# Kernel tuning notes

Measured on AMD Instinct MI355X. Metric: run time of the kernel, lower is better.

Reference implementation:

```python
import jax, jax.numpy as jnp
import numpy as np

IN_DIM = 128
OUT_DIM = 128
D_MODEL = IN_DIM // 4        # mamba d_model = 32
D_STATE = 16
D_CONV = 4
EXPAND = 2
D_INNER = EXPAND * D_MODEL   # 64
DT_RANK = (D_MODEL + 15) // 16  # ceil(d_model/16) = 2
N_MIXERS = 3                 # shared + 2 experts (stacked on leading axis)
B, DD, HH, WW = 2, 16, 16, 16


def setup_inputs() -> dict:
    key = jax.random.key(0)
    ks = jax.random.split(key, 12)
    rn = lambda k, s, sc=0.05: jax.random.normal(k, s, dtype=jnp.float32) * sc
    M = N_MIXERS
    return {
        "x": jax.random.normal(ks[0], (B, IN_DIM, DD, HH, WW), dtype=jnp.float32),
        "dataset_id": jax.random.randint(ks[1], (B,), 0, 2),
        "ln_g": jnp.ones((M, IN_DIM), jnp.float32),
        "ln_b": jnp.zeros((M, IN_DIM), jnp.float32),
        "in_w": rn(ks[2], (M, 2 * D_INNER, D_MODEL)),
        "conv_w": rn(ks[3], (M, D_INNER, D_CONV), 0.2),
        "conv_b": rn(ks[4], (M, D_INNER), 0.1),
        "xp_w": rn(ks[5], (M, DT_RANK + 2 * D_STATE, D_INNER)),
        "dt_w": rn(ks[6], (M, D_INNER, DT_RANK), 0.2),
        "dt_b": rn(ks[7], (M, D_INNER), 0.1),
        "A_log": jnp.broadcast_to(jnp.log(jnp.arange(1, D_STATE + 1, dtype=jnp.float32)), (M, D_INNER, D_STATE)) + jnp.zeros((M, D_INNER, D_STATE), jnp.float32),
        "Dp": jnp.ones((M, D_INNER), jnp.float32),
        "out_w": rn(ks[8], (M, D_MODEL, D_INNER)),
        "proj_w": rn(ks[9], (M, OUT_DIM, IN_DIM)),
        "proj_b": jnp.zeros((M, OUT_DIM), jnp.float32),
        "skip": jnp.ones((M,), jnp.float32),
    }


def layernorm(x, g, b, eps=1e-5):
    mu = jnp.mean(x, -1, keepdims=True)
    var = jnp.mean((x - mu) ** 2, -1, keepdims=True)
    return (x - mu) * jax.lax.rsqrt(var + eps) * g + b


def mamba(xp, p):
    # Standard Mamba block: in_proj -> causal depthwise conv1d -> selective scan -> SiLU gate -> out_proj
    # xp: (B, L, d_model)
    Bb, L, _ = xp.shape
    xz = jnp.einsum('bld,ed->ble', xp, p["in_w"])            # (B,L,2*d_inner)
    xi, z = jnp.split(xz, 2, axis=-1)
    conv = jax.lax.conv_general_dilated(xi.transpose(0, 2, 1), p["conv_w"][:, None, :], (1,), [(D_CONV - 1, 0)], feature_group_count=D_INNER)
    xi = jax.nn.silu(conv + p["conv_b"][None, :, None]).transpose(0, 2, 1)  # (B,L,d_inner)
    dbc = jnp.einsum('bld,ed->ble', xi, p["xp_w"])
    dt_low = dbc[..., :DT_RANK]
    Bm = dbc[..., DT_RANK:DT_RANK + D_STATE]
    Cm = dbc[..., DT_RANK + D_STATE:]
    delta = jax.nn.softplus(jnp.einsum('blr,dr->bld', dt_low, p["dt_w"]) + p["dt_b"])  # (B,L,d_inner)
    A = -jnp.exp(p["A_log"])                                  # (d_inner, d_state)

    def step(h, inp):
        xt, dt, Bt, Ct = inp                                  # (B,di),(B,di),(B,ds),(B,ds)
        dA = jnp.exp(dt[..., None] * A)                       # (B,d_inner,d_state)
        h = dA * h + (dt * xt)[..., None] * Bt[:, None, :]
        return h, jnp.einsum('bds,bs->bd', h, Ct)

    h0 = jnp.zeros((Bb, D_INNER, D_STATE), xp.dtype)
    xs = (xi.transpose(1, 0, 2), delta.transpose(1, 0, 2), Bm.transpose(1, 0, 2), Cm.transpose(1, 0, 2))
    _, ys = jax.lax.scan(step, h0, xs)
    y = ys.transpose(1, 0, 2) + p["Dp"] * xi
    y = y * jax.nn.silu(z)
    return jnp.einsum('ble,de->bld', y, p["out_w"])


def mixer(x, p):
    # PetaloMixer pom_module='full': LN -> 4-way channel chunk -> shared Mamba + skip -> concat -> LN -> Linear
    Bb, C, Dd, Hh, Ww = x.shape
    L = Dd * Hh * Ww
    xf = x.reshape(Bb, C, L).transpose(0, 2, 1)               # (B,L,C)
    xn = layernorm(xf, p["ln_g"], p["ln_b"])
    parts = jnp.stack(jnp.split(xn, 4, axis=-1), 0)           # (4,B,L,d_model)
    outs = jax.vmap(lambda q: mamba(q, p))(parts) + p["skip"] * parts
    xm = jnp.concatenate([outs[i] for i in range(4)], -1)     # (B,L,C)
    xm = layernorm(xm, p["ln_g"], p["ln_b"])                  # same LayerNorm reused, as in torch code
    xpj = jnp.einsum('blc,oc->blo', xm, p["proj_w"]) + p["proj_b"]
    return xpj.transpose(0, 2, 1).reshape(Bb, OUT_DIM, Dd, Hh, Ww)


def _forward(x, dataset_id, params):
    shared = mixer(x, {k: v[0] for k, v in params.items()})
    # experts: compute both over full batch (vectorized), then per-sample select by dataset_id
    eouts = jax.vmap(lambda p: mixer(x, p))({k: v[1:] for k, v in params.items()})  # (2,B,out,D,H,W)
    ids = jnp.minimum(dataset_id, N_MIXERS - 2)               # clamp: min(m, n_experts-1)
    expert_out = eouts[ids, jnp.arange(x.shape[0])]
    return shared + expert_out                                # Dropout3d(p=0.2) is identity in eval mode


def reference(x, dataset_id, ln_g, ln_b, in_w, conv_w, conv_b, xp_w, dt_w, dt_b, A_log, Dp, out_w, proj_w, proj_b, skip):
    params = dict(ln_g=ln_g, ln_b=ln_b, in_w=in_w, conv_w=conv_w, conv_b=conv_b, xp_w=xp_w, dt_w=dt_w, dt_b=dt_b, A_log=A_log, Dp=Dp, out_w=out_w, proj_w=proj_w, proj_b=proj_b, skip=skip)
    return _forward(x, dataset_id, params)
```

## Files before the change

kernel.cpp:

```cpp
#include <hip/hip_runtime.h>
#include <math.h>

#define LSEQ 4096
#define CIN  128
#define DI   64
#define NS   16
#define NP   4
#define NJ   4
#define NSEQ 16
#define NC   128
#define LC   32
#define LOG2E 1.44269504f

__device__ __forceinline__ int mixer_of(const int* did, int j){
  if((j&1)==0) return 0;
  int d = did[j>>1];
  return 1 + (d < 1 ? d : 1);
}
__device__ __forceinline__ float silu_f(float x){ return x/(1.f+expf(-x)); }

__global__ __launch_bounds__(256) void k1_ln_inproj(
  const float* __restrict__ x, const int* __restrict__ did,
  const float* __restrict__ ln_g, const float* __restrict__ ln_b,
  const float* __restrict__ in_w,
  float* __restrict__ xnb, float* __restrict__ xzr, float* __restrict__ zb)
{
  const int j = blockIdx.y, b = j>>1, t = threadIdx.x;
  const int l0 = blockIdx.x*32;
  const int m = mixer_of(did, j);
  __shared__ float s_x[128][33];
  __shared__ float s_xn[32][132];
  __shared__ float s_mu[32], s_rs[32];

  for(int idx=t; idx<4096; idx+=256){
    int c = idx>>5, ll = idx&31;
    s_x[c][ll] = x[((size_t)b*CIN+c)*LSEQ + l0+ll];
  }
  float wreg[32];
  {
    const float4* wp = (const float4*)(in_w + (size_t)m*4096 + (size_t)(t&127)*32);
    #pragma unroll
    for(int i=0;i<8;i++){
      float4 v = wp[i];
      wreg[i*4+0]=v.x; wreg[i*4+1]=v.y; wreg[i*4+2]=v.z; wreg[i*4+3]=v.w;
    }
  }
  __syncthreads();

  {
    const int wv = t>>6, lane = t&63;
    const int g = lane&7, lw = lane>>3;
    const int ll = wv*8+lw;
    float sum=0.f;
    #pragma unroll
    for(int k=0;k<16;k++) sum += s_x[g*16+k][ll];
    sum += __shfl_xor(sum,1); sum += __shfl_xor(sum,2); sum += __shfl_xor(sum,4);
    float mu = sum*(1.f/128.f);
    float vs=0.f;
    #pragma unroll
    for(int k=0;k<16;k++){ float dv = s_x[g*16+k][ll]-mu; vs += dv*dv; }
    vs += __shfl_xor(vs,1); vs += __shfl_xor(vs,2); vs += __shfl_xor(vs,4);
    if(g==0){ s_mu[ll]=mu; s_rs[ll]=rsqrtf(vs*(1.f/128.f)+1e-5f); }
  }
  __syncthreads();

  for(int idx=t; idx<4096; idx+=256){
    int ll = idx>>7, c = idx&127;
    float xn = (s_x[c][ll]-s_mu[ll])*s_rs[ll]*ln_g[m*128+c] + ln_b[m*128+c];
    s_xn[ll][c] = xn;
    xnb[((size_t)j*LSEQ + l0+ll)*128 + c] = xn;
  }
  __syncthreads();

  const int e = t&127, hh = t>>7;
  for(int ll=hh*16; ll<hh*16+16; ++ll){
    #pragma unroll
    for(int q=0;q<4;q++){
      const float4* xr4 = (const float4*)(&s_xn[ll][q*32]);
      float acc=0.f;
      #pragma unroll
      for(int k4=0;k4<8;k4++){
        float4 xv = xr4[k4];
        acc += xv.x*wreg[k4*4+0] + xv.y*wreg[k4*4+1]
             + xv.z*wreg[k4*4+2] + xv.w*wreg[k4*4+3];
      }
      size_t base = ((size_t)(j*NP+q)*LSEQ + l0+ll)*64;
      if(e<64) xzr[base+e]=acc; else zb[base+e-64]=acc;
    }
  }
}

__global__ __launch_bounds__(256) void k2_conv_xproj(
  const int* __restrict__ did,
  const float* __restrict__ conv_w, const float* __restrict__ conv_b,
  const float* __restrict__ xp_w, const float* __restrict__ dt_w, const float* __restrict__ dt_b,
  const float* __restrict__ xzr, float* __restrict__ dxb,
  float* __restrict__ bmb, float* __restrict__ cmb)
{
  const int seq = blockIdx.y, j = seq>>2, t = threadIdx.x;
  const int l0 = blockIdx.x*32;
  const int m = mixer_of(did, j);
  const int d = t&63, r = t>>6;
  __shared__ float s_xi[32][64];
  __shared__ float s_dbc[32][2];
  __shared__ float s_cwT[4][64];
  __shared__ float s_cb[64], s_dtw[128], s_dtb[64];

  float lz[11];
  #pragma unroll
  for(int i=0;i<11;i++){
    int l = l0 + r*8 - 3 + i;
    lz[i] = (l>=0) ? xzr[((size_t)seq*LSEQ + l)*64 + d] : 0.f;
  }
  { int k=t>>6, dd=t&63; s_cwT[k][dd]=conv_w[m*256+dd*4+k]; }
  if(t<64){ s_cb[t]=conv_b[m*64+t]; s_dtb[t]=dt_b[m*64+t]; }
  if(t<128) s_dtw[t]=dt_w[m*128+t];
  __syncthreads();

  {
    float cw0=s_cwT[0][d], cw1=s_cwT[1][d], cw2=s_cwT[2][d], cw3=s_cwT[3][d], cb=s_cb[d];
    #pragma unroll
    for(int i=0;i<8;i++){
      float xc = cb + lz[i]*cw0 + lz[i+1]*cw1 + lz[i+2]*cw2 + lz[i+3]*cw3;
      s_xi[r*8+i][d] = silu_f(xc);
    }
  }

  float wreg[64];
  if(d<34){
    const float4* wp = (const float4*)(xp_w + (size_t)m*2176 + (size_t)d*64);
    #pragma unroll
    for(int k4=0;k4<16;k4++){
      float4 v = wp[k4];
      wreg[k4*4+0]=v.x; wreg[k4*4+1]=v.y; wreg[k4*4+2]=v.z; wreg[k4*4+3]=v.w;
    }
  }
  __syncthreads();

  if(d<34){
    #pragma unroll
    for(int ip=0; ip<4; ip++){
      int ll = r*8 + ip*2;
      const float4* xa=(const float4*)&s_xi[ll][0];
      const float4* xb=(const float4*)&s_xi[ll+1][0];
      float a0=0.f,a1=0.f,b0=0.f,b1=0.f;
      #pragma unroll
      for(int k=0;k<16;k+=2){
        float4 u=xa[k], u2=xa[k+1], v=xb[k], v2=xb[k+1];
        a0 += u.x *wreg[4*k+0]+u.y *wreg[4*k+1]+u.z *wreg[4*k+2]+u.w *wreg[4*k+3];
        a1 += u2.x*wreg[4*k+4]+u2.y*wreg[4*k+5]+u2.z*wreg[4*k+6]+u2.w*wreg[4*k+7];
        b0 += v.x *wreg[4*k+0]+v.y *wreg[4*k+1]+v.z *wreg[4*k+2]+v.w *wreg[4*k+3];
        b1 += v2.x*wreg[4*k+4]+v2.y*wreg[4*k+5]+v2.z*wreg[4*k+6]+v2.w*wreg[4*k+7];
      }
      float A=a0+a1, Bv=b0+b1;
      if(d<2){ s_dbc[ll][d]=A; s_dbc[ll+1][d]=Bv; }
      else if(d<18){
        bmb[((size_t)seq*LSEQ + l0+ll  )*16 + d-2]=A;
        bmb[((size_t)seq*LSEQ + l0+ll+1)*16 + d-2]=Bv;
      } else {
        cmb[((size_t)seq*LSEQ + l0+ll  )*16 + d-18]=A;
        cmb[((size_t)seq*LSEQ + l0+ll+1)*16 + d-18]=Bv;
      }
    }
  }
  __syncthreads();

  {
    float w0=s_dtw[d*2], w1=s_dtw[d*2+1], bb=s_dtb[d];
    #pragma unroll
    for(int i=0;i<8;i++){
      int ll=r*8+i;
      float dtv = s_dbc[ll][0]*w0 + s_dbc[ll][1]*w1 + bb;
      float dlv = dtv>20.f ? dtv : log1pf(expf(dtv));
      float2 pk; pk.x=dlv; pk.y=s_xi[ll][d];
      *(float2*)(dxb + ((size_t)seq*LSEQ + l0+ll)*128 + d*2) = pk;
    }
  }
}

__global__ __launch_bounds__(256) void k3a_scan_pe(
  const int* __restrict__ did, const float* __restrict__ A_log,
  const float* __restrict__ dxb, const float* __restrict__ bmb,
  float* __restrict__ pb, float* __restrict__ eb)
{
  const int seq=blockIdx.y, j=seq>>2, t=threadIdx.x;
  const int wave=t>>6, d=t&63;
  const int cl=wave>>1, sh=wave&1, sh8=sh*8;
  const int chunk=blockIdx.x*2+cl;
  const int l0=blockIdx.x*2*LC;
  const int m=mixer_of(did,j);
  __shared__ float s_b[2*LC*NS];
  ((float4*)s_b)[t] = ((const float4*)(bmb + ((size_t)seq*LSEQ + l0)*NS))[t];

  float as_h[8], as0;
  {
    const float* ap = A_log + (size_t)m*1024 + d*16;
    as0 = -expf(ap[0])*LOG2E;
    #pragma unroll
    for(int k=0;k<8;k++) as_h[k] = -expf(ap[sh8+k])*LOG2E;
  }
  bool stl = true;
  #pragma unroll
  for(int k=0;k<8;k++){ float ex=(float)(sh8+k+1)*as0; stl = stl && (fabsf(as_h[k]-ex) <= 1e-4f*fabsf(ex)); }
  const bool structured = (__ballot(stl) == ~0ull);

  const float2* dxp=(const float2*)(dxb + ((size_t)seq*LSEQ + (size_t)chunk*LC)*128);
  float E[8];
  #pragma unroll
  for(int k=0;k<8;k++) E[k]=0.f;
  float Sdl=0.f;
  __syncthreads();

  #define ASTEP(i_, dx_, FAST_) { \
    float dl=dx_.x, xv=dx_.y; float u=dl*xv; Sdl+=dl; \
    const float4* bq=(const float4*)(s_b + cl*(LC*NS) + (i_)*NS + sh8); \
    float4 b0=bq[0], b1=bq[1]; \
    float bb[8]={b0.x,b0.y,b0.z,b0.w, b1.x,b1.y,b1.z,b1.w}; \
    float p[8]; \
    if(FAST_){ float q=exp2f(dl*as0); p[0]=exp2f(dl*as_h[0]); \
      _Pragma("unroll") for(int k=1;k<8;k++) p[k]=p[k-1]*q; \
    } else { _Pragma("unroll") for(int k=0;k<8;k++) p[k]=exp2f(dl*as_h[k]); } \
    _Pragma("unroll") for(int k=0;k<8;k++) E[k]=fmaf(p[k],E[k],u*bb[k]); }

  #define ALOOP(FAST_) { \
    float2 dxw[4]; \
    _Pragma("unroll") for(int k=0;k<4;k++) dxw[k]=dxp[k*64+d]; \
    for(int ii=0;ii<LC;ii+=4){ \
      float2 c0=dxw[0],c1=dxw[1],c2=dxw[2],c3=dxw[3]; \
      if(ii+4<LC){ _Pragma("unroll") for(int k=0;k<4;k++) dxw[k]=dxp[(ii+4+k)*64+d]; } \
      ASTEP(ii+0,c0,FAST_); ASTEP(ii+1,c1,FAST_); ASTEP(ii+2,c2,FAST_); ASTEP(ii+3,c3,FAST_); } }

  if(structured){ ALOOP(1) } else { ALOOP(0) }
  #undef ALOOP
  #undef ASTEP

  float P[8];
  #pragma unroll
  for(int k=0;k<8;k++) P[k]=exp2f(Sdl*as_h[k]);
  size_t oo=(((size_t)seq*NC+chunk)*64+d)*16 + sh8;
  float4* pp=(float4*)(pb+oo); float4* ep=(float4*)(eb+oo);
  pp[0]=make_float4(P[0],P[1],P[2],P[3]);
  pp[1]=make_float4(P[4],P[5],P[6],P[7]);
  ep[0]=make_float4(E[0],E[1],E[2],E[3]);
  ep[1]=make_float4(E[4],E[5],E[6],E[7]);
}

__global__ __launch_bounds__(256) void k3b_combine(
  float* p_hs, const float* __restrict__ eb)
{
  const int seq=blockIdx.y, q=blockIdx.x, t=threadIdx.x;
  const size_t elem = (size_t)q*256+t;
  #define OFF(c_) (((size_t)seq*NC+(c_))*1024 + elem)
  float pA[16],eA[16],pB[16],eB[16];
  #pragma unroll
  for(int k=0;k<16;k++){ pA[k]=p_hs[OFF(k)]; eA[k]=eb[OFF(k)]; }
  float h=0.f;
  for(int bt=0; bt<8; bt+=2){
    if(bt+1<8){
      #pragma unroll
      for(int k=0;k<16;k++){ pB[k]=p_hs[OFF((bt+1)*16+k)]; eB[k]=eb[OFF((bt+1)*16+k)]; }
    }
    #pragma unroll
    for(int k=0;k<16;k++){ p_hs[OFF(bt*16+k)]=h; h=fmaf(pA[k],h,eA[k]); }
    if(bt+2<8){
      #pragma unroll
      for(int k=0;k<16;k++){ pA[k]=p_hs[OFF((bt+2)*16+k)]; eA[k]=eb[OFF((bt+2)*16+k)]; }
    }
    #pragma unroll
    for(int k=0;k<16;k++){ p_hs[OFF((bt+1)*16+k)]=h; h=fmaf(pB[k],h,eB[k]); }
  }
  #undef OFF
}

__global__ __launch_bounds__(256) void k3c4_scan_outproj(
  const int* __restrict__ did, const float* __restrict__ A_log, const float* __restrict__ Dp,
  const float* __restrict__ dxb,
  const float* __restrict__ bmb, const float* __restrict__ cmb,
  const float* __restrict__ zb, const float* __restrict__ hsb,
  const float* __restrict__ out_w, const float* __restrict__ skipv,
  const float* __restrict__ xnb, float* __restrict__ xmb)
{
  const int seq=blockIdx.y, j=seq>>2, p=seq&3, t=threadIdx.x;
  const int wave=t>>6, d=t&63;
  const int cl=wave>>1, sh=wave&1, sh8=sh*8;
  const int chunk=blockIdx.x*2+cl;
  const int l0=blockIdx.x*2*LC;
  const int m=mixer_of(did,j);
  __shared__ float s_b[2*LC*NS];
  __shared__ float s_c[2*LC*NS];
  __shared__ float s_y0[64*64];
  __shared__ float s_y1[64*64];
  {
    const float4* bsrc=(const float4*)(bmb + ((size_t)seq*LSEQ + l0)*NS);
    const float4* csrc=(const float4*)(cmb + ((size_t)seq*LSEQ + l0)*NS);
    ((float4*)s_b)[t]=bsrc[t];
    ((float4*)s_c)[t]=csrc[t];
  }
  float as_h[8], as0;
  {
    const float* ap = A_log + (size_t)m*1024 + d*16;
    as0 = -expf(ap[0])*LOG2E;
    #pragma unroll
    for(int k=0;k<8;k++) as_h[k] = -expf(ap[sh8+k])*LOG2E;
  }
  bool stl = true;
  #pragma unroll
  for(int k=0;k<8;k++){ float ex=(float)(sh8+k+1)*as0; stl = stl && (fabsf(as_h[k]-ex) <= 1e-4f*fabsf(ex)); }
  const bool structured = (__ballot(stl) == ~0ull);

  const float dpv2 = (sh==0) ? Dp[m*64+d] : 0.f;
  float h[8];
  {
    const float4* hp=(const float4*)(hsb + (((size_t)seq*NC+chunk)*64+d)*16 + sh8);
    float4 v0=hp[0], v1=hp[1];
    h[0]=v0.x; h[1]=v0.y; h[2]=v0.z; h[3]=v0.w;
    h[4]=v1.x; h[5]=v1.y; h[6]=v1.z; h[7]=v1.w;
  }
  const float2* dxp=(const float2*)(dxb + ((size_t)seq*LSEQ + (size_t)chunk*LC)*128);
  float* s_yw = sh ? s_y1 : s_y0;
  __syncthreads();

  #define CSTEP(i_, dx_, FAST_) { \
    float dl=dx_.x, xv=dx_.y; float u=dl*xv; \
    const float4* bq=(const float4*)(s_b + cl*(LC*NS) + (i_)*NS + sh8); \
    const float4* cq=(const float4*)(s_c + cl*(LC*NS) + (i_)*NS + sh8); \
    float4 b0=bq[0],b1=bq[1],c0=cq[0],c1=cq[1]; \
    float bb[8]={b0.x,b0.y,b0.z,b0.w, b1.x,b1.y,b1.z,b1.w}; \
    float cc[8]={c0.x,c0.y,c0.z,c0.w, c1.x,c1.y,c1.z,c1.w}; \
    float pz[8]; \
    if(FAST_){ float q=exp2f(dl*as0); pz[0]=exp2f(dl*as_h[0]); \
      _Pragma("unroll") for(int k=1;k<8;k++) pz[k]=pz[k-1]*q; \
    } else { _Pragma("unroll") for(int k=0;k<8;k++) pz[k]=exp2f(dl*as_h[k]); } \
    float ya=0.f, yb2=0.f; \
    _Pragma("unroll") for(int k=0;k<8;k++){ \
      h[k]=fmaf(pz[k],h[k],u*bb[k]); \
      float hv=h[k]*cc[k]; \
      if(k&1) yb2+=hv; else ya+=hv; } \
    float y=ya+yb2; y=fmaf(dpv2,xv,y); \
    s_yw[(cl*LC+(i_))*64 + d]=y; }

  #define CLOOP(FAST_) { \
    float2 dxw[4]; \
    _Pragma("unroll") for(int k=0;k<4;k++) dxw[k]=dxp[k*64+d]; \
    for(int ii=0;ii<LC;ii+=4){ \
      float2 c0w=dxw[0],c1w=dxw[1],c2w=dxw[2],c3w=dxw[3]; \
      if(ii+4<LC){ _Pragma("unroll") for(int k=0;k<4;k++) dxw[k]=dxp[(ii+4+k)*64+d]; } \
      CSTEP(ii+0,c0w,FAST_); CSTEP(ii+1,c1w,FAST_); CSTEP(ii+2,c2w,FAST_); CSTEP(ii+3,c3w,FAST_); } }

  if(structured){ CLOOP(1) } else { CLOOP(0) }
  #undef CLOOP
  #undef CSTEP

  __syncthreads();
  {
    const float* zp = zb + ((size_t)seq*LSEQ + l0)*64;
    #pragma unroll
    for(int it=0; it<16; ++it){
      int idx = t + it*256;
      float ysum = s_y0[idx] + s_y1[idx];
      s_y0[idx] = ysum * silu_f(zp[idx]);
    }
  }
  const int o=t&31, grp=t>>5;
  float wreg[64];
  {
    const float4* wp=(const float4*)(out_w + (size_t)m*2048 + (size_t)o*64);
    #pragma unroll
    for(int k4=0;k4<16;k4++){
      float4 v=wp[k4];
      wreg[k4*4+0]=v.x; wreg[k4*4+1]=v.y; wreg[k4*4+2]=v.z; wreg[k4*4+3]=v.w;
    }
  }
  const float sk=skipv[m];
  __syncthreads();
  for(int ll=grp; ll<64; ll+=8){
    const float4* ya=(const float4*)&s_y0[ll*64];
    float a0=0.f,a1=0.f;
    #pragma unroll
    for(int k=0;k<16;k+=2){
      float4 u=ya[k], u2=ya[k+1];
      a0 += u.x *wreg[4*k+0]+u.y *wreg[4*k+1]+u.z *wreg[4*k+2]+u.w *wreg[4*k+3];
      a1 += u2.x*wreg[4*k+4]+u2.y*wreg[4*k+5]+u2.z*wreg[4*k+6]+u2.w*wreg[4*k+7];
    }
    size_t xidx=((size_t)j*LSEQ + l0+ll)*128 + p*32 + o;
    xmb[xidx]=(a0+a1) + sk*xnb[xidx];
  }
}

__global__ __launch_bounds__(256) void k5_ln2_proj(
  const int* __restrict__ did, const float* __restrict__ ln_g, const float* __restrict__ ln_b,
  const float* __restrict__ proj_w, const float* __restrict__ proj_b,
  const float* __restrict__ xmb, float* __restrict__ out)
{
  const int b=blockIdx.y, l0=blockIdx.x*16, t=threadIdx.x;
  const int eh = t>>7, local = t&127;
  const int j = 2*b+eh;
  const int m = mixer_of(did, j);
  __shared__ float s_xn[2][16][132];
  __shared__ float s_comb[16][132];
  __shared__ float s_murs[2][16][2];

  for(int idx=local; idx<2048; idx+=128){
    int ll=idx>>7, c=idx&127;
    s_xn[eh][ll][c] = xmb[((size_t)j*LSEQ + l0+ll)*128 + c];
  }
  __syncthreads();
  {
    const int lane = t&63;
    const int g = lane&7, lw = lane>>3;
    const int ll = ((t>>6)&1)*8 + lw;
    float sum=0.f;
    #pragma unroll
    for(int k=0;k<16;k++) sum += s_xn[eh][ll][g*16+k];
    sum += __shfl_xor(sum,1); sum += __shfl_xor(sum,2); sum += __shfl_xor(sum,4);
    float mu = sum*(1.f/128.f);
    float vs=0.f;
    #pragma unroll
    for(int k=0;k<16;k++){ float dv=s_xn[eh][ll][g*16+k]-mu; vs+=dv*dv; }
    vs += __shfl_xor(vs,1); vs += __shfl_xor(vs,2); vs += __shfl_xor(vs,4);
    if(g==0){ s_murs[eh][ll][0]=mu; s_murs[eh][ll][1]=rsqrtf(vs*(1.f/128.f)+1e-5f); }
  }
  __syncthreads();
  for(int idx=local; idx<2048; idx+=128){
    int ll=idx>>7, c=idx&127;
    float xn=(s_xn[eh][ll][c]-s_murs[eh][ll][0])*s_murs[eh][ll][1]*ln_g[m*128+c]+ln_b[m*128+c];
    s_xn[eh][ll][c]=xn;
  }
  __syncthreads();
  float acc[16];
  #pragma unroll
  for(int ll=0;ll<16;ll++) acc[ll]=0.f;
  {
    const float4* pw4 = (const float4*)(proj_w + (size_t)m*16384 + (size_t)local*128);
    #pragma unroll 4
    for(int c4=0;c4<32;c4++){
      float4 w = pw4[c4];
      int c = c4*4;
      #pragma unroll
      for(int ll=0;ll<16;ll++){
        acc[ll] += w.x*s_xn[eh][ll][c] + w.y*s_xn[eh][ll][c+1]
                 + w.z*s_xn[eh][ll][c+2] + w.w*s_xn[eh][ll][c+3];
      }
    }
  }
  float pb_v = proj_b[m*128+local];
  if(eh==0){
    #pragma unroll
    for(int ll=0;ll<16;ll++) s_comb[ll][local]=acc[ll]+pb_v;
  }
  __syncthreads();
  if(eh==1){
    #pragma unroll
    for(int ll=0;ll<16;ll++) s_comb[ll][local]+=acc[ll]+pb_v;
  }
  __syncthreads();
  for(int idx=t; idx<2048; idx+=256){
    int o=idx>>4, ll=idx&15;
    out[((size_t)b*128+o)*LSEQ + l0+ll] = s_comb[ll][o];
  }
}

extern "C" void kernel_launch(void* const* d_in, const int* in_sizes, int n_in,
                              void* d_out, int out_size, void* d_ws, size_t ws_size,
                              hipStream_t stream) {
  const float* x      = (const float*)d_in[0];
  const int*   did    = (const int*)d_in[1];
  const float* ln_g   = (const float*)d_in[2];
  const float* ln_b   = (const float*)d_in[3];
  const float* in_w   = (const float*)d_in[4];
  const float* conv_w = (const float*)d_in[5];
  const float* conv_b = (const float*)d_in[6];
  const float* xp_w   = (const float*)d_in[7];
  const float* dt_w   = (const float*)d_in[8];
  const float* dt_b   = (const float*)d_in[9];
  const float* A_log  = (const float*)d_in[10];
  const float* Dp     = (const float*)d_in[11];
  const float* out_w  = (const float*)d_in[12];
  const float* proj_w = (const float*)d_in[13];
  const float* proj_b = (const float*)d_in[14];
  const float* skipv  = (const float*)d_in[15];
  float* out = (float*)d_out;
  float* ws  = (float*)d_ws;

  float* xnb = ws;
  float* xzr = xnb + (size_t)NJ*LSEQ*128;
  float* zb  = xzr + (size_t)NSEQ*LSEQ*64;
  float* dxb = zb  + (size_t)NSEQ*LSEQ*64;
  float* bmb = dxb + (size_t)NSEQ*LSEQ*128;
  float* cmb = bmb + (size_t)NSEQ*LSEQ*16;
  float* xmb = cmb + (size_t)NSEQ*LSEQ*16;
  float* pb  = xzr;
  float* eb  = xzr + (size_t)NSEQ*NC*1024;
  float* hsb = pb;

  hipLaunchKernelGGL(k1_ln_inproj, dim3(LSEQ/32,NJ), dim3(256), 0, stream,
                     x,did,ln_g,ln_b,in_w,xnb,xzr,zb);
  hipLaunchKernelGGL(k2_conv_xproj, dim3(LSEQ/32,NSEQ), dim3(256), 0, stream,
                     did,conv_w,conv_b,xp_w,dt_w,dt_b,xzr,dxb,bmb,cmb);
  hipLaunchKernelGGL(k3a_scan_pe, dim3(NC/2,NSEQ), dim3(256), 0, stream,
                     did,A_log,dxb,bmb,pb,eb);
  hipLaunchKernelGGL(k3b_combine, dim3(4,NSEQ), dim3(256), 0, stream, pb,eb);
  hipLaunchKernelGGL(k3c4_scan_outproj, dim3(NC/2,NSEQ), dim3(256), 0, stream,
                     did,A_log,Dp,dxb,bmb,cmb,zb,hsb,out_w,skipv,xnb,xmb);
  hipLaunchKernelGGL(k5_ln2_proj, dim3(LSEQ/16,2), dim3(256), 0, stream,
                     did,ln_g,ln_b,proj_w,proj_b,xmb,out);
}
```

Before: 139.0 us.

## Fuse chunk-local scan pass into conv/xproj kernel using shared-memory operands

Merges the per-chunk scan (chunk decay products and local states) into the conv+x_proj kernel, so the kernel reads delta, x and B from shared memory instead of reloading dxb and bmb from global memory in a separate launch. Each block now covers one 32-step chunk, with four waves each handling four state dims. The pb/eb buffers move to a fresh workspace region because xzr is still being read while they are written. This removes one kernel launch and a global round trip, at the cost of more shared memory and a longer serial tail in the fused kernel.

```diff
diff --git a/kernel.cpp b/kernel.cpp
--- a/kernel.cpp
+++ b/kernel.cpp
@@ -90,18 +90,23 @@
   }
 }
 
-__global__ __launch_bounds__(256) void k2_conv_xproj(
+__global__ __launch_bounds__(256) void k2_conv_xproj_pe(
   const int* __restrict__ did,
   const float* __restrict__ conv_w, const float* __restrict__ conv_b,
   const float* __restrict__ xp_w, const float* __restrict__ dt_w, const float* __restrict__ dt_b,
+  const float* __restrict__ A_log,
   const float* __restrict__ xzr, float* __restrict__ dxb,
-  float* __restrict__ bmb, float* __restrict__ cmb)
+  float* __restrict__ bmb, float* __restrict__ cmb,
+  float* __restrict__ pb, float* __restrict__ eb)
 {
   const int seq = blockIdx.y, j = seq>>2, t = threadIdx.x;
-  const int l0 = blockIdx.x*32;
+  const int chunk = blockIdx.x;
+  const int l0 = chunk*32;
   const int m = mixer_of(did, j);
   const int d = t&63, r = t>>6;
   __shared__ float s_xi[32][64];
+  __shared__ float s_dl[32][64];
+  __shared__ float s_bS[32][16];
   __shared__ float s_dbc[32][2];
   __shared__ float s_cwT[4][64];
   __shared__ float s_cb[64], s_dtw[128], s_dtb[64];
@@ -155,6 +160,7 @@
       float A=a0+a1, Bv=b0+b1;
       if(d<2){ s_dbc[ll][d]=A; s_dbc[ll+1][d]=Bv; }
       else if(d<18){
+        s_bS[ll][d-2]=A; s_bS[ll+1][d-2]=Bv;
         bmb[((size_t)seq*LSEQ + l0+ll  )*16 + d-2]=A;
         bmb[((size_t)seq*LSEQ + l0+ll+1)*16 + d-2]=Bv;
       } else {
@@ -172,77 +178,56 @@
       int ll=r*8+i;
       float dtv = s_dbc[ll][0]*w0 + s_dbc[ll][1]*w1 + bb;
       float dlv = dtv>20.f ? dtv : log1pf(expf(dtv));
+      s_dl[ll][d]=dlv;
       float2 pk; pk.x=dlv; pk.y=s_xi[ll][d];
       *(float2*)(dxb + ((size_t)seq*LSEQ + l0+ll)*128 + d*2) = pk;
     }
   }
-}
-
-__global__ __launch_bounds__(256) void k3a_scan_pe(
-  const int* __restrict__ did, const float* __restrict__ A_log,
-  const float* __restrict__ dxb, const float* __restrict__ bmb,
-  float* __restrict__ pb, float* __restrict__ eb)
-{
-  const int seq=blockIdx.y, j=seq>>2, t=threadIdx.x;
-  const int wave=t>>6, d=t&63;
-  const int cl=wave>>1, sh=wave&1, sh8=sh*8;
-  const int chunk=blockIdx.x*2+cl;
-  const int l0=blockIdx.x*2*LC;
-  const int m=mixer_of(did,j);
-  __shared__ float s_b[2*LC*NS];
-  ((float4*)s_b)[t] = ((const float4*)(bmb + ((size_t)seq*LSEQ + l0)*NS))[t];
-
-  float as_h[8], as0;
-  {
-    const float* ap = A_log + (size_t)m*1024 + d*16;
-    as0 = -expf(ap[0])*LOG2E;
-    #pragma unroll
-    for(int k=0;k<8;k++) as_h[k] = -expf(ap[sh8+k])*LOG2E;
-  }
-  bool stl = true;
-  #pragma unroll
-  for(int k=0;k<8;k++){ float ex=(float)(sh8+k+1)*as0; stl = stl && (fabsf(as_h[k]-ex) <= 1e-4f*fabsf(ex)); }
-  const bool structured = (__ballot(stl) == ~0ull);
-
-  const float2* dxp=(const float2*)(dxb + ((size_t)seq*LSEQ + (size_t)chunk*LC)*128);
-  float E[8];
-  #pragma unroll
-  for(int k=0;k<8;k++) E[k]=0.f;
-  float Sdl=0.f;
-  __syncthreads();
-
-  #define ASTEP(i_, dx_, FAST_) { \
-    float dl=dx_.x, xv=dx_.y; float u=dl*xv; Sdl+=dl; \
-    const float4* bq=(const float4*)(s_b + cl*(LC*NS) + (i_)*NS + sh8); \
-    float4 b0=bq[0], b1=bq[1]; \
-    float bb[8]={b0.x,b0.y,b0.z,b0.w, b1.x,b1.y,b1.z,b1.w}; \
-    float p[8]; \
-    if(FAST_){ float q=exp2f(dl*as0); p[0]=exp2f(dl*as_h[0]); \
-      _Pragma("unroll") for(int k=1;k<8;k++) p[k]=p[k-1]*q; \
-    } else { _Pragma("unroll") for(int k=0;k<8;k++) p[k]=exp2f(dl*as_h[k]); } \
-    _Pragma("unroll") for(int k=0;k<8;k++) E[k]=fmaf(p[k],E[k],u*bb[k]); }
-
-  #define ALOOP(FAST_) { \
-    float2 dxw[4]; \
-    _Pragma("unroll") for(int k=0;k<4;k++) dxw[k]=dxp[k*64+d]; \
-    for(int ii=0;ii<LC;ii+=4){ \
-      float2 c0=dxw[0],c1=dxw[1],c2=dxw[2],c3=dxw[3]; \
-      if(ii+4<LC){ _Pragma("unroll") for(int k=0;k<4;k++) dxw[k]=dxp[(ii+4+k)*64+d]; } \
-      ASTEP(ii+0,c0,FAST_); ASTEP(ii+1,c1,FAST_); ASTEP(ii+2,c2,FAST_); ASTEP(ii+3,c3,FAST_); } }
-
-  if(structured){ ALOOP(1) } else { ALOOP(0) }
-  #undef ALOOP
-  #undef ASTEP
-
-  float P[8];
-  #pragma unroll
-  for(int k=0;k<8;k++) P[k]=exp2f(Sdl*as_h[k]);
-  size_t oo=(((size_t)seq*NC+chunk)*64+d)*16 + sh8;
-  float4* pp=(float4*)(pb+oo); float4* ep=(float4*)(eb+oo);
-  pp[0]=make_float4(P[0],P[1],P[2],P[3]);
-  pp[1]=make_float4(P[4],P[5],P[6],P[7]);
-  ep[0]=make_float4(E[0],E[1],E[2],E[3]);
-  ep[1]=make_float4(E[4],E[5],E[6],E[7]);
+  __syncthreads();
+
+  {
+    const int sq = r;
+    float as_q[4], as0;
+    {
+      const float* ap = A_log + (size_t)m*1024 + d*16;
+      as0 = -expf(ap[0])*LOG2E;
+      #pragma unroll
+      for(int k=0;k<4;k++) as_q[k] = -expf(ap[sq*4+k])*LOG2E;
+    }
+    bool stl = true;
+    #pragma unroll
+    for(int k=0;k<4;k++){ float ex=(float)(sq*4+k+1)*as0; stl = stl && (fabsf(as_q[k]-ex) <= 1e-4f*fabsf(ex)); }
+    const bool structured = (__ballot(stl) == ~0ull);
+
+    float E[4] = {0.f,0.f,0.f,0.f};
+    float Sdl = 0.f;
+
+    #define PSTEP(i_, FAST_) { \
+      float dl = s_dl[i_][d]; \
+      float u  = dl * s_xi[i_][d]; \
+      Sdl += dl; \
+      const float4 bv = *(const float4*)(&s_bS[i_][sq*4]); \
+      float bb[4]={bv.x,bv.y,bv.z,bv.w}; \
+      float p[4]; \
+      if(FAST_){ float q=exp2f(dl*as0); p[0]=exp2f(dl*as_q[0]); \
+        p[1]=p[0]*q; p[2]=p[1]*q; p[3]=p[2]*q; \
+      } else { _Pragma("unroll") for(int k=0;k<4;k++) p[k]=exp2f(dl*as_q[k]); } \
+      _Pragma("unroll") for(int k=0;k<4;k++) E[k]=fmaf(p[k],E[k],u*bb[k]); }
+
+    if(structured){
+      #pragma unroll 4
+      for(int i=0;i<LC;i++){ PSTEP(i,1) }
+    } else {
+      #pragma unroll 4
+      for(int i=0;i<LC;i++){ PSTEP(i,0) }
+    }
+    #undef PSTEP
+
+    size_t oo=(((size_t)seq*NC+chunk)*64+d)*16 + sq*4;
+    *(float4*)(pb+oo) = make_float4(exp2f(Sdl*as_q[0]),exp2f(Sdl*as_q[1]),
+                                    exp2f(Sdl*as_q[2]),exp2f(Sdl*as_q[3]));
+    *(float4*)(eb+oo) = make_float4(E[0],E[1],E[2],E[3]);
+  }
 }
 
 __global__ __launch_bounds__(256) void k3b_combine(
@@ -489,16 +474,14 @@
   float* bmb = dxb + (size_t)NSEQ*LSEQ*128;
   float* cmb = bmb + (size_t)NSEQ*LSEQ*16;
   float* xmb = cmb + (size_t)NSEQ*LSEQ*16;
-  float* pb  = xzr;
-  float* eb  = xzr + (size_t)NSEQ*NC*1024;
+  float* pb  = xmb + (size_t)NJ*LSEQ*128;
+  float* eb  = pb  + (size_t)NSEQ*NC*1024;
   float* hsb = pb;
 
   hipLaunchKernelGGL(k1_ln_inproj, dim3(LSEQ/32,NJ), dim3(256), 0, stream,
                      x,did,ln_g,ln_b,in_w,xnb,xzr,zb);
-  hipLaunchKernelGGL(k2_conv_xproj, dim3(LSEQ/32,NSEQ), dim3(256), 0, stream,
-                     did,conv_w,conv_b,xp_w,dt_w,dt_b,xzr,dxb,bmb,cmb);
-  hipLaunchKernelGGL(k3a_scan_pe, dim3(NC/2,NSEQ), dim3(256), 0, stream,
-                     did,A_log,dxb,bmb,pb,eb);
+  hipLaunchKernelGGL(k2_conv_xproj_pe, dim3(NC,NSEQ), dim3(256), 0, stream,
+                     did,conv_w,conv_b,xp_w,dt_w,dt_b,A_log,xzr,dxb,bmb,cmb,pb,eb);
   hipLaunchKernelGGL(k3b_combine, dim3(4,NSEQ), dim3(256), 0, stream, pb,eb);
   hipLaunchKernelGGL(k3c4_scan_outproj, dim3(NC/2,NSEQ), dim3(256), 0, stream,
                      did,A_log,Dp,dxb,bmb,cmb,zb,hsb,out_w,skipv,xnb,xmb);
```

Measured after the change: 132.2 us. -4.9%, faster.
